# Performance work log

Measured on AMD Instinct MI355X. Metric: run time of the kernel, lower is better.

Reference implementation:

```python
import jax, jax.numpy as jnp
import numpy as np

N_NODES = 50000
N_EDGES = 800000
IN_CH = 128
HEADS = 4
HID = 32  # per-head dim; heads*hid = 128
N_GRAPHS = 128


def setup_inputs() -> dict:
    key = jax.random.key(0)
    ks = jax.random.split(key, 32)
    d = {}
    d["x"] = jax.random.normal(ks[0], (N_NODES, IN_CH), dtype=jnp.float32)
    d["edge_index"] = jax.random.randint(ks[1], (2, N_EDGES), 0, N_NODES, dtype=jnp.int64)
    d["batch"] = jnp.sort(jax.random.randint(ks[2], (N_NODES,), 0, N_GRAPHS, dtype=jnp.int64))
    HD = HEADS * HID
    names = [("wq1", (IN_CH, HD)), ("bq1", (HD,)), ("wk1", (IN_CH, HD)), ("bk1", (HD,)),
             ("wv1", (IN_CH, HD)), ("bv1", (HD,)), ("ws1", (IN_CH, HD)), ("bs1", (HD,)),
             ("wq2", (HD, HD)), ("bq2", (HD,)), ("wk2", (HD, HD)), ("bk2", (HD,)),
             ("wv2", (HD, HD)), ("bv2", (HD,)), ("ws2", (HD, HD)), ("bs2", (HD,)),
             ("wl", (HD, HD)), ("bl", (HD,)), ("wl2", (HD, 1)), ("bl2", (1,))]
    for i, (nm, shp) in enumerate(names):
        d[nm] = jax.random.normal(ks[3 + i], shp, dtype=jnp.float32) * 0.05
    return d


def _transformer_conv(x, src, dst, wq, bq, wk, bk, wv, bv, ws, bs):
    """PyG TransformerConv: multi-head dot-product attention over edges,
    softmax normalized per destination node, plus linear root/skip term."""
    N = x.shape[0]
    q = (x @ wq + bq).reshape(N, HEADS, HID)
    k = (x @ wk + bk).reshape(N, HEADS, HID)
    v = (x @ wv + bv).reshape(N, HEADS, HID)
    # edge scores: [E, H]
    e = jnp.einsum('ehd,ehd->eh', q[dst], k[src]) * np.float32(1.0 / np.sqrt(HID))
    # segment softmax over incoming edges of each destination node
    m = jax.ops.segment_max(e, dst, num_segments=N)
    a = jnp.exp(e - m[dst])
    s = jax.ops.segment_sum(a, dst, num_segments=N)
    alpha = a / s[dst]  # [E, H]
    msg = alpha[:, :, None] * v[src]  # [E, H, D]
    out = jax.ops.segment_sum(msg, dst, num_segments=N).reshape(N, HEADS * HID)
    return out + x @ ws + bs  # root weight (skip) term


def reference(x, edge_index, batch,
              wq1, bq1, wk1, bk1, wv1, bv1, ws1, bs1,
              wq2, bq2, wk2, bk2, wv2, bv2, ws2, bs2,
              wl, bl, wl2, bl2):
    src, dst = edge_index[0], edge_index[1]
    h = _transformer_conv(x, src, dst, wq1, bq1, wk1, bk1, wv1, bv1, ws1, bs1)
    h = jax.nn.relu(h)
    h = _transformer_conv(h, src, dst, wq2, bq2, wk2, bk2, wv2, bv2, ws2, bs2)
    h = jax.nn.relu(h)
    h = h @ wl + bl
    h = h @ wl2 + bl2  # [N, 1]
    # global mean pool over graphs
    sums = jax.ops.segment_sum(h, batch, num_segments=N_GRAPHS)
    cnts = jax.ops.segment_sum(jnp.ones((h.shape[0], 1), h.dtype), batch, num_segments=N_GRAPHS)
    return sums / jnp.maximum(cnts, 1.0)
```

## Files before the change

kernel.cpp:

```cpp
#include <hip/hip_runtime.h>
#include <hip/hip_bf16.h>
#include <math.h>

#define NNODES 50000
#define NEDGES 800000
#define NGRAPHS 128
#define SCAN_B ((NNODES + 255) / 256)

typedef __attribute__((ext_vector_type(8))) short bf16x8;
typedef __attribute__((ext_vector_type(4))) float f32x4;

__device__ __forceinline__ unsigned short f2bf(float f) {
    unsigned int u = __float_as_uint(f);
    return (unsigned short)((u + 0x7FFFu + ((u >> 16) & 1u)) >> 16);
}
__device__ __forceinline__ unsigned pack2bf(float a, float b) {
    return (unsigned)f2bf(a) | ((unsigned)f2bf(b) << 16);
}
__device__ __forceinline__ float2 bf2f2(unsigned int u) {
    float2 f;
    f.x = __uint_as_float(u << 16);
    f.y = __uint_as_float(u & 0xFFFF0000u);
    return f;
}

__global__ void count_edges(const int* __restrict__ ei, int* __restrict__ cnt) {
    int e = blockIdx.x * 256 + threadIdx.x;
    if (e < NEDGES) atomicAdd(&cnt[ei[NEDGES + e]], 1);
}

__global__ __launch_bounds__(256)
void scan_pass1(const int* __restrict__ cnt, int* __restrict__ bsum) {
    const int t = threadIdx.x;
    const int i = blockIdx.x * 256 + t;
    int v = (i < NNODES) ? cnt[i] : 0;
#pragma unroll
    for (int off = 32; off > 0; off >>= 1) v += __shfl_xor(v, off, 64);
    __shared__ int ws[4];
    if ((t & 63) == 0) ws[t >> 6] = v;
    __syncthreads();
    if (t == 0) bsum[blockIdx.x] = ws[0] + ws[1] + ws[2] + ws[3];
}

__global__ __launch_bounds__(256)
void scan_pass2(const int* __restrict__ bsum, int* __restrict__ boff) {
    const int t = threadIdx.x;
    const int v = (t < SCAN_B) ? bsum[t] : 0;
    __shared__ int a[256];
    a[t] = v;
    __syncthreads();
    for (int off = 1; off < 256; off <<= 1) {
        const int u = (t >= off) ? a[t - off] : 0;
        __syncthreads();
        a[t] += u;
        __syncthreads();
    }
    if (t < SCAN_B) boff[t] = a[t] - v;
}

__global__ __launch_bounds__(256)
void scan_pass3(const int* __restrict__ cnt, const int* __restrict__ boff,
                int* __restrict__ rowptr, int* __restrict__ wpos) {
    const int t = threadIdx.x;
    const int i = blockIdx.x * 256 + t;
    const int v = (i < NNODES) ? cnt[i] : 0;
    __shared__ int a[256];
    a[t] = v;
    __syncthreads();
    for (int off = 1; off < 256; off <<= 1) {
        const int u = (t >= off) ? a[t - off] : 0;
        __syncthreads();
        a[t] += u;
        __syncthreads();
    }
    if (i < NNODES) {
        const int e = boff[blockIdx.x] + a[t] - v;
        rowptr[i] = e;
        wpos[i]   = e;
    }
    if (i == 0) rowptr[NNODES] = NEDGES;
}

__global__ void fill_csr(const int* __restrict__ ei, int* __restrict__ wpos,
                         int* __restrict__ colsrc) {
    int e = blockIdx.x * 256 + threadIdx.x;
    if (e < NEDGES) {
        int d = ei[NEDGES + e];
        int slot = atomicAdd(&wpos[d], 1);
        colsrc[slot] = ei[e];
    }
}

__global__ __launch_bounds__(64)
void fuse_wl(const float* __restrict__ wl, const float* __restrict__ bl,
             const float* __restrict__ wl2, const float* __restrict__ bl2,
             float* __restrict__ wf, float* __restrict__ bf) {
    const int g = blockIdx.x;
    const int l = threadIdx.x;
    const float* row = (g < 128) ? &wl[g * 128] : bl;
    float s = row[l] * wl2[l] + row[64 + l] * wl2[64 + l];
#pragma unroll
    for (int off = 32; off > 0; off >>= 1) s += __shfl_xor(s, off, 64);
    if (l == 0) {
        if (g < 128) wf[g] = s;
        else         bf[0] = s + bl2[0];
    }
}

__global__ void prep_w(const float* __restrict__ wq1, const float* __restrict__ wk1,
                       const float* __restrict__ wv1, const float* __restrict__ ws1,
                       const float* __restrict__ wq2, const float* __restrict__ wk2,
                       const float* __restrict__ wv2, const float* __restrict__ ws2,
                       unsigned short* __restrict__ Wt) {
    const int layer = blockIdx.z;
    const int sel   = blockIdx.y;
    const float* W = layer == 0
        ? (sel == 0 ? wq1 : sel == 1 ? wk1 : sel == 2 ? wv1 : ws1)
        : (sel == 0 ? wq2 : sel == 1 ? wk2 : sel == 2 ? wv2 : ws2);
    const int idx = blockIdx.x * 256 + threadIdx.x;
    const int col = idx & 127;
    const int k   = idx >> 7;
    Wt[layer * 65536 + sel * 16384 + col * 128 + k] = f2bf(W[k * 128 + col]);
}

template <bool A_BF16>
__global__ __launch_bounds__(256)
void gemm_qkvs(const void* __restrict__ Fv, const unsigned short* __restrict__ Wt,
               const float* __restrict__ bq, const float* __restrict__ bk,
               const float* __restrict__ bv, const float* __restrict__ bsk,
               unsigned short* __restrict__ Qb, unsigned short* __restrict__ Kb,
               unsigned short* __restrict__ Vb, unsigned short* __restrict__ Hb) {
    __shared__ __align__(16) unsigned short As[128][136];
    __shared__ __align__(16) unsigned short Bt[2][64][136];
    const int t    = threadIdx.x;
    const int m0   = blockIdx.x * 128;
    const int lane = t & 63;
    const int w    = t >> 6;
    const int l15  = lane & 15;
    const int lg   = lane >> 4;

    {
        const int row = t >> 1;
        const int kh  = (t & 1) * 64;
        const int gr  = min(m0 + row, NNODES - 1);
        if constexpr (A_BF16) {
            const unsigned short* src = &((const unsigned short*)Fv)[(size_t)gr * 128 + kh];
#pragma unroll
            for (int p = 0; p < 8; ++p)
                *(uint4*)&As[row][kh + p * 8] = *(const uint4*)&src[p * 8];
        } else {
            const float* src = &((const float*)Fv)[(size_t)gr * 128 + kh];
#pragma unroll
            for (int p = 0; p < 16; ++p) {
                const float4 v = *(const float4*)&src[p * 4];
                ushort4 u;
                u.x = f2bf(v.x); u.y = f2bf(v.y); u.z = f2bf(v.z); u.w = f2bf(v.w);
                *(ushort4*)&As[row][kh + p * 4] = u;
            }
        }
    }

#define STAGE_B(BUF, SL)                                                       \
    {                                                                          \
        const int sel_ = (SL) >> 1, c0_ = ((SL) & 1) * 64;                     \
        const int col = t >> 2, kb = (t & 3) * 32;                             \
        const unsigned short* src = &Wt[sel_ * 16384 + (c0_ + col) * 128 + kb];\
        _Pragma("unroll")                                                      \
        for (int p = 0; p < 4; ++p)                                            \
            *(uint4*)&Bt[BUF][col][kb + p * 8] = *(const uint4*)&src[p * 8];   \
    }

    STAGE_B(0, 0)
    __syncthreads();

    for (int sl = 0; sl < 8; ++sl) {
        const int cur = sl & 1;
        if (sl < 7) STAGE_B(cur ^ 1, sl + 1)

        const int sel = sl >> 1;
        const int c0  = (sl & 1) * 64;
        const float* bias = sel == 0 ? bq : sel == 1 ? bk : sel == 2 ? bv : bsk;
        unsigned short* Ob = sel == 0 ? Qb : sel == 1 ? Kb : sel == 2 ? Vb : Hb;

        const float b0 = bias[c0 + l15];
        const float b1 = bias[c0 + 16 + l15];
        const float b2 = bias[c0 + 32 + l15];
        const float b3 = bias[c0 + 48 + l15];
        f32x4 a00 = {b0, b0, b0, b0}, a01 = {b1, b1, b1, b1},
              a02 = {b2, b2, b2, b2}, a03 = {b3, b3, b3, b3};
        f32x4 a10 = a00, a11 = a01, a12 = a02, a13 = a03;
#pragma unroll
        for (int ks = 0; ks < 4; ++ks) {
            const int kof = ks * 32 + lg * 8;
            const bf16x8 af0 = *(const bf16x8*)&As[w * 32 + l15][kof];
            const bf16x8 af1 = *(const bf16x8*)&As[w * 32 + 16 + l15][kof];
            const bf16x8 bf0 = *(const bf16x8*)&Bt[cur][l15][kof];
            const bf16x8 bf1 = *(const bf16x8*)&Bt[cur][16 + l15][kof];
            const bf16x8 bf2 = *(const bf16x8*)&Bt[cur][32 + l15][kof];
            const bf16x8 bf3 = *(const bf16x8*)&Bt[cur][48 + l15][kof];
            a00 = __builtin_amdgcn_mfma_f32_16x16x32_bf16(af0, bf0, a00, 0, 0, 0);
            a01 = __builtin_amdgcn_mfma_f32_16x16x32_bf16(af0, bf1, a01, 0, 0, 0);
            a02 = __builtin_amdgcn_mfma_f32_16x16x32_bf16(af0, bf2, a02, 0, 0, 0);
            a03 = __builtin_amdgcn_mfma_f32_16x16x32_bf16(af0, bf3, a03, 0, 0, 0);
            a10 = __builtin_amdgcn_mfma_f32_16x16x32_bf16(af1, bf0, a10, 0, 0, 0);
            a11 = __builtin_amdgcn_mfma_f32_16x16x32_bf16(af1, bf1, a11, 0, 0, 0);
            a12 = __builtin_amdgcn_mfma_f32_16x16x32_bf16(af1, bf2, a12, 0, 0, 0);
            a13 = __builtin_amdgcn_mfma_f32_16x16x32_bf16(af1, bf3, a13, 0, 0, 0);
        }

        const int r0 = m0 + w * 32 + lg * 4;
#define STB(ACC, RT, CT)                                                       \
        _Pragma("unroll")                                                      \
        for (int i = 0; i < 4; ++i) {                                          \
            const int gr = r0 + (RT) * 16 + i;                                 \
            if (gr < NNODES)                                                   \
                Ob[(size_t)gr * 128 + c0 + (CT) * 16 + l15] = f2bf(ACC[i]);    \
        }
        STB(a00, 0, 0) STB(a01, 0, 1) STB(a02, 0, 2) STB(a03, 0, 3)
        STB(a10, 1, 0) STB(a11, 1, 1) STB(a12, 1, 2) STB(a13, 1, 3)
#undef STB
        __syncthreads();
    }
#undef STAGE_B
}

template <bool FUSE_HEAD>
__global__ __launch_bounds__(128)
void attn_agg(const unsigned short* __restrict__ Qb,
              const unsigned short* __restrict__ Kb,
              const unsigned short* __restrict__ Vb,
              unsigned short* __restrict__ Hb,
              const int* __restrict__ rowptr, const int* __restrict__ colsrc,
              const float* __restrict__ wf, float* __restrict__ r) {
    const int n = blockIdx.x * 2 + (threadIdx.x >> 6);
    const int l = threadIdx.x & 63;
    const int e = l >> 4;
    const int c = (l & 15) * 8;
    const uint4 qu = *(const uint4*)&Qb[(size_t)n * 128 + c];
    const float S = 0.17677669529663687f * 1.4426950408889634f;
    const float2 t01 = bf2f2(qu.x), t23 = bf2f2(qu.y);
    const float2 t45 = bf2f2(qu.z), t67 = bf2f2(qu.w);
    const float q0 = t01.x * S, q1 = t01.y * S, q2 = t23.x * S, q3 = t23.y * S;
    const float q4 = t45.x * S, q5 = t45.y * S, q6 = t67.x * S, q7 = t67.y * S;
    const int beg = rowptr[n], end = rowptr[n + 1];
    const int cnt = end - beg;

    float m = -INFINITY, s = 0.f;
    float a0 = 0.f, a1 = 0.f, a2 = 0.f, a3 = 0.f;
    float a4 = 0.f, a5 = 0.f, a6 = 0.f, a7 = 0.f;

    uint4 ku, vu;
    if (cnt > 0) {
        const int src = colsrc[min(beg + e, end - 1)];
        ku = *(const uint4*)&Kb[(size_t)src * 128 + c];
        vu = *(const uint4*)&Vb[(size_t)src * 128 + c];
    }
    for (int i = beg; i < end; i += 4) {
        const uint4 kc = ku, vc = vu;
        const bool valid = (i + e) < end;
        if (i + 4 < end) {
            const int srcN = colsrc[min(i + 4 + e, end - 1)];
            ku = *(const uint4*)&Kb[(size_t)srcN * 128 + c];
            vu = *(const uint4*)&Vb[(size_t)srcN * 128 + c];
        }
        const float2 k01 = bf2f2(kc.x), k23 = bf2f2(kc.y);
        const float2 k45 = bf2f2(kc.z), k67 = bf2f2(kc.w);
        float p = q0 * k01.x;
        p = fmaf(q1, k01.y, p); p = fmaf(q2, k23.x, p); p = fmaf(q3, k23.y, p);
        p = fmaf(q4, k45.x, p); p = fmaf(q5, k45.y, p); p = fmaf(q6, k67.x, p);
        p = fmaf(q7, k67.y, p);
        p += __shfl_xor(p, 2);
        p += __shfl_xor(p, 1);
        if (!valid) p = -INFINITY;
        if (!__all(p <= m + 8.f)) {
            float pm = fmaxf(p, __shfl_xor(p, 16));
            pm = fmaxf(pm, __shfl_xor(pm, 32));
            const float nm = fmaxf(m, pm);
            const float sc = exp2f(m - nm);
            s *= sc;
            a0 *= sc; a1 *= sc; a2 *= sc; a3 *= sc;
            a4 *= sc; a5 *= sc; a6 *= sc; a7 *= sc;
            m = nm;
        }
        const float w = exp2f(p - m);
        s += w;
        const float2 v01 = bf2f2(vc.x), v23 = bf2f2(vc.y);
        const float2 v45 = bf2f2(vc.z), v67 = bf2f2(vc.w);
        a0 = fmaf(w, v01.x, a0); a1 = fmaf(w, v01.y, a1);
        a2 = fmaf(w, v23.x, a2); a3 = fmaf(w, v23.y, a3);
        a4 = fmaf(w, v45.x, a4); a5 = fmaf(w, v45.y, a5);
        a6 = fmaf(w, v67.x, a6); a7 = fmaf(w, v67.y, a7);
    }
    s  += __shfl_xor(s, 16);  s  += __shfl_xor(s, 32);
    a0 += __shfl_xor(a0, 16); a0 += __shfl_xor(a0, 32);
    a1 += __shfl_xor(a1, 16); a1 += __shfl_xor(a1, 32);
    a2 += __shfl_xor(a2, 16); a2 += __shfl_xor(a2, 32);
    a3 += __shfl_xor(a3, 16); a3 += __shfl_xor(a3, 32);
    a4 += __shfl_xor(a4, 16); a4 += __shfl_xor(a4, 32);
    a5 += __shfl_xor(a5, 16); a5 += __shfl_xor(a5, 32);
    a6 += __shfl_xor(a6, 16); a6 += __shfl_xor(a6, 32);
    a7 += __shfl_xor(a7, 16); a7 += __shfl_xor(a7, 32);

    const uint4 hu = *(const uint4*)&Hb[(size_t)n * 128 + c];
    const float2 h01 = bf2f2(hu.x), h23 = bf2f2(hu.y);
    const float2 h45 = bf2f2(hu.z), h67 = bf2f2(hu.w);
    float o0 = h01.x, o1 = h01.y, o2 = h23.x, o3 = h23.y;
    float o4 = h45.x, o5 = h45.y, o6 = h67.x, o7 = h67.y;
    if (cnt > 0) {
        const float inv = 1.f / s;
        o0 = fmaf(a0, inv, o0); o1 = fmaf(a1, inv, o1);
        o2 = fmaf(a2, inv, o2); o3 = fmaf(a3, inv, o3);
        o4 = fmaf(a4, inv, o4); o5 = fmaf(a5, inv, o5);
        o6 = fmaf(a6, inv, o6); o7 = fmaf(a7, inv, o7);
    }
    o0 = fmaxf(o0, 0.f); o1 = fmaxf(o1, 0.f); o2 = fmaxf(o2, 0.f);
    o3 = fmaxf(o3, 0.f); o4 = fmaxf(o4, 0.f); o5 = fmaxf(o5, 0.f);
    o6 = fmaxf(o6, 0.f); o7 = fmaxf(o7, 0.f);
    if (!FUSE_HEAD) {
        if (e == 0) {
            uint4 o;
            o.x = pack2bf(o0, o1); o.y = pack2bf(o2, o3);
            o.z = pack2bf(o4, o5); o.w = pack2bf(o6, o7);
            *(uint4*)&Hb[(size_t)n * 128 + c] = o;
        }
    } else {
        const float4 wA = *(const float4*)&wf[c];
        const float4 wB = *(const float4*)&wf[c + 4];
        float val = fmaf(o0, wA.x, fmaf(o1, wA.y, fmaf(o2, wA.z, o3 * wA.w)));
        val = fmaf(o4, wB.x, fmaf(o5, wB.y, fmaf(o6, wB.z, fmaf(o7, wB.w, val))));
        val += __shfl_xor(val, 8);
        val += __shfl_xor(val, 4);
        val += __shfl_xor(val, 2);
        val += __shfl_xor(val, 1);
        if (l == 0) r[n] = val;
    }
}

__global__ __launch_bounds__(256)
void graph_pool(const float* __restrict__ r, const int* __restrict__ batch,
                const float* __restrict__ bf, float* __restrict__ out) {
    const int g = blockIdx.x;
    const int t = threadIdx.x;
    int lo = 0, hi = NNODES;
    while (lo < hi) { int mid = (lo + hi) >> 1; if (batch[mid] < g) lo = mid + 1; else hi = mid; }
    const int beg = lo;
    lo = beg; hi = NNODES;
    while (lo < hi) { int mid = (lo + hi) >> 1; if (batch[mid] < g + 1) lo = mid + 1; else hi = mid; }
    const int end = lo;

    float s = 0.f;
    for (int i = beg + t; i < end; i += 256) s += r[i];
#pragma unroll
    for (int off = 32; off > 0; off >>= 1) s += __shfl_xor(s, off, 64);
    __shared__ float pw[4];
    if ((t & 63) == 0) pw[t >> 6] = s;
    __syncthreads();
    if (t == 0) {
        const float cnt = (float)(end - beg);
        const float tot = pw[0] + pw[1] + pw[2] + pw[3] + cnt * bf[0];
        out[g] = tot / fmaxf(cnt, 1.f);
    }
}

extern "C" void kernel_launch(void* const* d_in, const int* in_sizes, int n_in,
                              void* d_out, int out_size, void* d_ws, size_t ws_size,
                              hipStream_t stream) {
    const float* x     = (const float*)d_in[0];
    const int*   ei    = (const int*)d_in[1];
    const int*   batch = (const int*)d_in[2];
    const float* wq1 = (const float*)d_in[3];  const float* bq1 = (const float*)d_in[4];
    const float* wk1 = (const float*)d_in[5];  const float* bk1 = (const float*)d_in[6];
    const float* wv1 = (const float*)d_in[7];  const float* bv1 = (const float*)d_in[8];
    const float* ws1 = (const float*)d_in[9];  const float* bs1 = (const float*)d_in[10];
    const float* wq2 = (const float*)d_in[11]; const float* bq2 = (const float*)d_in[12];
    const float* wk2 = (const float*)d_in[13]; const float* bk2 = (const float*)d_in[14];
    const float* wv2 = (const float*)d_in[15]; const float* bv2 = (const float*)d_in[16];
    const float* ws2 = (const float*)d_in[17]; const float* bs2 = (const float*)d_in[18];
    const float* wl  = (const float*)d_in[19]; const float* bl  = (const float*)d_in[20];
    const float* wl2 = (const float*)d_in[21]; const float* bl2 = (const float*)d_in[22];

    char* wsb = (char*)d_ws;
    size_t off = 0;
    auto carve = [&](size_t bytes) -> void* {
        void* p = wsb + off;
        off = (off + bytes + 255) & ~(size_t)255;
        return p;
    };
    const size_t NB = (size_t)NNODES * 128 * 2;
    unsigned short* Qb = (unsigned short*)carve(NB);
    unsigned short* Kb = (unsigned short*)carve(NB);
    unsigned short* Vb = (unsigned short*)carve(NB);
    unsigned short* H1 = (unsigned short*)carve(NB);
    unsigned short* H2 = (unsigned short*)carve(NB);
    int*   rowptr = (int*)carve((NNODES + 1) * sizeof(int));
    int*   wpos   = (int*)carve(NNODES * sizeof(int));
    int*   cnt    = (int*)carve(NNODES * sizeof(int));
    int*   colsrc = (int*)carve(NEDGES * sizeof(int));
    int*   bsum   = (int*)carve(256 * sizeof(int));
    int*   boff   = (int*)carve(256 * sizeof(int));
    float* wf     = (float*)carve(129 * sizeof(float));
    float* bf     = wf + 128;
    float* nodeval = (float*)carve(NNODES * sizeof(float));
    unsigned short* Wt = (unsigned short*)carve(131072 * sizeof(unsigned short));

    hipMemsetAsync(cnt, 0, NNODES * sizeof(int), stream);

    count_edges<<<(NEDGES + 255) / 256, 256, 0, stream>>>(ei, cnt);
    scan_pass1<<<SCAN_B, 256, 0, stream>>>(cnt, bsum);
    scan_pass2<<<1, 256, 0, stream>>>(bsum, boff);
    scan_pass3<<<SCAN_B, 256, 0, stream>>>(cnt, boff, rowptr, wpos);
    fill_csr<<<(NEDGES + 255) / 256, 256, 0, stream>>>(ei, wpos, colsrc);
    fuse_wl<<<129, 64, 0, stream>>>(wl, bl, wl2, bl2, wf, bf);
    prep_w<<<dim3(64, 4, 2), 256, 0, stream>>>(wq1, wk1, wv1, ws1,
                                               wq2, wk2, wv2, ws2, Wt);

    const int ggrid = (NNODES + 127) / 128;
    const int agrid = NNODES / 2;
    gemm_qkvs<false><<<ggrid, 256, 0, stream>>>(x, Wt, bq1, bk1, bv1, bs1,
                                                Qb, Kb, Vb, H1);
    attn_agg<false><<<agrid, 128, 0, stream>>>(Qb, Kb, Vb, H1, rowptr, colsrc,
                                               nullptr, nullptr);
    gemm_qkvs<true><<<ggrid, 256, 0, stream>>>(H1, Wt + 65536, bq2, bk2, bv2, bs2,
                                               Qb, Kb, Vb, H2);
    attn_agg<true><<<agrid, 128, 0, stream>>>(Qb, Kb, Vb, H2, rowptr, colsrc,
                                              wf, nodeval);
    graph_pool<<<NGRAPHS, 256, 0, stream>>>(nodeval, batch, bf, (float*)d_out);
}
```

Before: 369.6 us.

## Read GEMM weights directly from global, drop LDS B staging, merge prep kernels

```diff
diff --git a/kernel.cpp b/kernel.cpp
--- a/kernel.cpp
+++ b/kernel.cpp
@@ -91,47 +91,50 @@
     }
 }
 
-__global__ __launch_bounds__(64)
-void fuse_wl(const float* __restrict__ wl, const float* __restrict__ bl,
-             const float* __restrict__ wl2, const float* __restrict__ bl2,
-             float* __restrict__ wf, float* __restrict__ bf) {
-    const int g = blockIdx.x;
-    const int l = threadIdx.x;
-    const float* row = (g < 128) ? &wl[g * 128] : bl;
-    float s = row[l] * wl2[l] + row[64 + l] * wl2[64 + l];
-#pragma unroll
-    for (int off = 32; off > 0; off >>= 1) s += __shfl_xor(s, off, 64);
-    if (l == 0) {
-        if (g < 128) wf[g] = s;
-        else         bf[0] = s + bl2[0];
-    }
-}
-
-__global__ void prep_w(const float* __restrict__ wq1, const float* __restrict__ wk1,
-                       const float* __restrict__ wv1, const float* __restrict__ ws1,
-                       const float* __restrict__ wq2, const float* __restrict__ wk2,
-                       const float* __restrict__ wv2, const float* __restrict__ ws2,
-                       unsigned short* __restrict__ Wt) {
-    const int layer = blockIdx.z;
-    const int sel   = blockIdx.y;
-    const float* W = layer == 0
-        ? (sel == 0 ? wq1 : sel == 1 ? wk1 : sel == 2 ? wv1 : ws1)
-        : (sel == 0 ? wq2 : sel == 1 ? wk2 : sel == 2 ? wv2 : ws2);
-    const int idx = blockIdx.x * 256 + threadIdx.x;
-    const int col = idx & 127;
-    const int k   = idx >> 7;
-    Wt[layer * 65536 + sel * 16384 + col * 128 + k] = f2bf(W[k * 128 + col]);
+__global__ __launch_bounds__(256)
+void prep_all(const float* __restrict__ wq1, const float* __restrict__ wk1,
+              const float* __restrict__ wv1, const float* __restrict__ ws1,
+              const float* __restrict__ wq2, const float* __restrict__ wk2,
+              const float* __restrict__ wv2, const float* __restrict__ ws2,
+              const float* __restrict__ wl, const float* __restrict__ bl,
+              const float* __restrict__ wl2, const float* __restrict__ bl2,
+              unsigned short* __restrict__ Wt, float* __restrict__ wf,
+              float* __restrict__ bf) {
+    const int b = blockIdx.x;
+    if (b < 512) {
+        const int layer = b >> 8;
+        const int sel   = (b >> 6) & 3;
+        const float* W = layer == 0
+            ? (sel == 0 ? wq1 : sel == 1 ? wk1 : sel == 2 ? wv1 : ws1)
+            : (sel == 0 ? wq2 : sel == 1 ? wk2 : sel == 2 ? wv2 : ws2);
+        const int idx = (b & 63) * 256 + threadIdx.x;
+        const int col = idx & 127;
+        const int k   = idx >> 7;
+        Wt[layer * 65536 + sel * 16384 + col * 128 + k] = f2bf(W[k * 128 + col]);
+    } else {
+        const int g = (b - 512) * 4 + (threadIdx.x >> 6);
+        const int l = threadIdx.x & 63;
+        if (g <= 128) {
+            const float* row = (g < 128) ? &wl[g * 128] : bl;
+            float s = row[l] * wl2[l] + row[64 + l] * wl2[64 + l];
+#pragma unroll
+            for (int off = 32; off > 0; off >>= 1) s += __shfl_xor(s, off, 64);
+            if (l == 0) {
+                if (g < 128) wf[g] = s;
+                else         bf[0] = s + bl2[0];
+            }
+        }
+    }
 }
 
 template <bool A_BF16>
-__global__ __launch_bounds__(256)
+__global__ __launch_bounds__(256, 3)
 void gemm_qkvs(const void* __restrict__ Fv, const unsigned short* __restrict__ Wt,
                const float* __restrict__ bq, const float* __restrict__ bk,
                const float* __restrict__ bv, const float* __restrict__ bsk,
                unsigned short* __restrict__ Qb, unsigned short* __restrict__ Kb,
                unsigned short* __restrict__ Vb, unsigned short* __restrict__ Hb) {
     __shared__ __align__(16) unsigned short As[128][136];
-    __shared__ __align__(16) unsigned short Bt[2][64][136];
     const int t    = threadIdx.x;
     const int m0   = blockIdx.x * 128;
     const int lane = t & 63;
@@ -159,28 +162,14 @@
             }
         }
     }
-
-#define STAGE_B(BUF, SL)                                                       \
-    {                                                                          \
-        const int sel_ = (SL) >> 1, c0_ = ((SL) & 1) * 64;                     \
-        const int col = t >> 2, kb = (t & 3) * 32;                             \
-        const unsigned short* src = &Wt[sel_ * 16384 + (c0_ + col) * 128 + kb];\
-        _Pragma("unroll")                                                      \
-        for (int p = 0; p < 4; ++p)                                            \
-            *(uint4*)&Bt[BUF][col][kb + p * 8] = *(const uint4*)&src[p * 8];   \
-    }
-
-    STAGE_B(0, 0)
     __syncthreads();
 
     for (int sl = 0; sl < 8; ++sl) {
-        const int cur = sl & 1;
-        if (sl < 7) STAGE_B(cur ^ 1, sl + 1)
-
         const int sel = sl >> 1;
         const int c0  = (sl & 1) * 64;
         const float* bias = sel == 0 ? bq : sel == 1 ? bk : sel == 2 ? bv : bsk;
         unsigned short* Ob = sel == 0 ? Qb : sel == 1 ? Kb : sel == 2 ? Vb : Hb;
+        const unsigned short* Wsel = Wt + sel * 16384 + (size_t)c0 * 128;
 
         const float b0 = bias[c0 + l15];
         const float b1 = bias[c0 + 16 + l15];
@@ -194,10 +183,10 @@
             const int kof = ks * 32 + lg * 8;
             const bf16x8 af0 = *(const bf16x8*)&As[w * 32 + l15][kof];
             const bf16x8 af1 = *(const bf16x8*)&As[w * 32 + 16 + l15][kof];
-            const bf16x8 bf0 = *(const bf16x8*)&Bt[cur][l15][kof];
-            const bf16x8 bf1 = *(const bf16x8*)&Bt[cur][16 + l15][kof];
-            const bf16x8 bf2 = *(const bf16x8*)&Bt[cur][32 + l15][kof];
-            const bf16x8 bf3 = *(const bf16x8*)&Bt[cur][48 + l15][kof];
+            const bf16x8 bf0 = *(const bf16x8*)&Wsel[(size_t)(l15) * 128 + kof];
+            const bf16x8 bf1 = *(const bf16x8*)&Wsel[(size_t)(16 + l15) * 128 + kof];
+            const bf16x8 bf2 = *(const bf16x8*)&Wsel[(size_t)(32 + l15) * 128 + kof];
+            const bf16x8 bf3 = *(const bf16x8*)&Wsel[(size_t)(48 + l15) * 128 + kof];
             a00 = __builtin_amdgcn_mfma_f32_16x16x32_bf16(af0, bf0, a00, 0, 0, 0);
             a01 = __builtin_amdgcn_mfma_f32_16x16x32_bf16(af0, bf1, a01, 0, 0, 0);
             a02 = __builtin_amdgcn_mfma_f32_16x16x32_bf16(af0, bf2, a02, 0, 0, 0);
@@ -219,9 +208,7 @@
         STB(a00, 0, 0) STB(a01, 0, 1) STB(a02, 0, 2) STB(a03, 0, 3)
         STB(a10, 1, 0) STB(a11, 1, 1) STB(a12, 1, 2) STB(a13, 1, 3)
 #undef STB
-        __syncthreads();
-    }
-#undef STAGE_B
+    }
 }
 
 template <bool FUSE_HEAD>
@@ -410,9 +397,8 @@
     scan_pass2<<<1, 256, 0, stream>>>(bsum, boff);
     scan_pass3<<<SCAN_B, 256, 0, stream>>>(cnt, boff, rowptr, wpos);
     fill_csr<<<(NEDGES + 255) / 256, 256, 0, stream>>>(ei, wpos, colsrc);
-    fuse_wl<<<129, 64, 0, stream>>>(wl, bl, wl2, bl2, wf, bf);
-    prep_w<<<dim3(64, 4, 2), 256, 0, stream>>>(wq1, wk1, wv1, ws1,
-                                               wq2, wk2, wv2, ws2, Wt);
+    prep_all<<<545, 256, 0, stream>>>(wq1, wk1, wv1, ws1, wq2, wk2, wv2, ws2,
+                                      wl, bl, wl2, bl2, Wt, wf, bf);
 
     const int ggrid = (NNODES + 127) / 128;
     const int agrid = NNODES / 2;
```

New measurement: 397.9 us. 1.08x slower.
